# Kernel tuning notes

Measured on AMD Instinct MI355X. Metric: run time of the kernel, lower is better.

## Reference

```python
import jax, jax.numpy as jnp
import numpy as np

BIN = 256      # bin_num
DELTA = 0.01   # Huber delta
IM = 256       # imSize


def _soft_hist(u):
    # u: [B,H,W] values in [0,1]; BiasedConv1 with weight=1, bias_k = -(-1 + 2k/BIN)
    bias = 1.0 - 2.0 * jnp.arange(BIN, dtype=u.dtype) / BIN          # [BIN]
    a1 = u[:, None, :, :] + bias[None, :, None, None]                # [B,BIN,H,W]
    return jax.nn.relu(1.0 - jnp.abs(a1) * (BIN - 1))                # triangular kernel


def _hist2d(img):
    # img: [B,2,H,W] in [-1,1]
    ha = _soft_hist((img[:, 0] + 1.0) / 2.0)                         # [B,BIN,H,W]
    hb = _soft_hist((img[:, 1] + 1.0) / 2.0)                         # [B,BIN,H,W]
    H, W = img.shape[2], img.shape[3]
    # torch: repeat/repeat-view + elementwise mul + AvgPool2d(imSize)
    # == per-pixel outer product of (hb, ha) averaged over all pixels:
    # hist2d[b, j, r] = mean_hw hb[b,j,h,w] * ha[b,r,h,w]
    h2 = jnp.einsum('bjhw,brhw->bjr', hb, ha) / (H * W)              # [B,BIN,BIN]
    return h2[:, None]                                               # [B,1,BIN,BIN]


def reference(inp_image, ref_image):
    h_inp = _hist2d(inp_image)
    h_gt = _hist2d(ref_image)
    mann = jnp.abs(h_inp - h_gt)
    eucl = 0.5 * mann ** 2
    mask = (mann < DELTA).astype(mann.dtype)
    loss = eucl * mask / DELTA + (mann - 0.5 * DELTA) * (1.0 - mask)
    return jnp.sum(loss, axis=1, keepdims=True)                      # [B,1,BIN,BIN]


def setup_inputs() -> dict:
    key = jax.random.key(0)
    k1, k2 = jax.random.split(key)
    inp = jax.random.uniform(k1, (2, 2, IM, IM), dtype=jnp.float32) * 2.0 - 1.0
    ref = jax.random.uniform(k2, (2, 2, IM, IM), dtype=jnp.float32) * 2.0 - 1.0
    return {"inp_image": inp, "ref_image": ref}
```

## Files before the change

kernel.cpp:

```cpp
#include <hip/hip_runtime.h>


#define NPIX 65536
#define BINS 256
#define REPL 4
#define HSZ  (2 * NPIX)

__global__ void __launch_bounds__(256)
scatter_kernel(const float* __restrict__ inp,
               const float* __restrict__ ref,
               float* __restrict__ hist) {
    int gid = blockIdx.x * blockDim.x + threadIdx.x;
    int pix = gid & (NPIX - 1);
    int bb  = (gid >> 16) & 1;
    int im  = gid >> 17;
    const float* src = im ? ref : inp;
    float sgn = im ? -1.f : 1.f;
    float x0 = src[bb * (2 * NPIX) + pix];
    float x1 = src[bb * (2 * NPIX) + NPIX + pix];
    float* h = hist + (blockIdx.x & (REPL - 1)) * HSZ + bb * (BINS * BINS);

    float t0 = 64.f * x0 + 192.f;
    float t1 = 64.f * x1 + 192.f;
    int k0 = (int)floorf(t0);
    int k1 = (int)floorf(t1);

    float wr[2]; int ir[2]; int nr = 0;
    #pragma unroll
    for (int d = 0; d < 2; ++d) {
        int k = k0 + d;
        float w = 1.f - fabsf(t0 - (float)k) * 1.9921875f;
        if (w > 0.f && k >= 0 && k < BINS) { wr[nr] = w; ir[nr] = k; ++nr; }
    }
    float wj[2]; int ij[2]; int nj = 0;
    #pragma unroll
    for (int d = 0; d < 2; ++d) {
        int k = k1 + d;
        float w = 1.f - fabsf(t1 - (float)k) * 1.9921875f;
        if (w > 0.f && k >= 0 && k < BINS) { wj[nj] = w * sgn; ij[nj] = k; ++nj; }
    }
    for (int a = 0; a < nj; ++a)
        for (int b = 0; b < nr; ++b)
            atomicAdd(&h[ij[a] * BINS + ir[b]], wj[a] * wr[b]);
}

__global__ void __launch_bounds__(256)
loss_rezero_kernel(float* __restrict__ hist,
                   float* __restrict__ out) {
    int idx = blockIdx.x * blockDim.x + threadIdx.x;
    int bb = idx >> 16;
    int jr = idx & (NPIX - 1);
    float s = 0.f;
    #pragma unroll
    for (int r = 0; r < REPL; ++r) {
        float* p = &hist[r * HSZ + bb * (BINS * BINS) + jr];
        s += *p;
        *p = 0.f;
    }
    const float inv = 1.f / 65536.f;
    float mann = fabsf(s) * inv;
    float loss = (mann < 0.01f) ? (50.f * mann * mann) : (mann - 0.005f);
    out[idx] = loss;
}

extern "C" void kernel_launch(void* const* d_in, const int* in_sizes, int n_in,
                              void* d_out, int out_size, void* d_ws, size_t ws_size,
                              hipStream_t stream) {
    const float* inp = (const float*)d_in[0];
    const float* ref = (const float*)d_in[1];
    float* hist = (float*)d_ws;
    float* out  = (float*)d_out;

    scatter_kernel<<<(4 * NPIX) / 256, 256, 0, stream>>>(inp, ref, hist);
    loss_rezero_kernel<<<(2 * NPIX) / 256, 256, 0, stream>>>(hist, out);
}
```

Baseline: 69.71 us.

## Fuse scatter and loss kernels with a global atomic-counter grid barrier

Merges the histogram scatter and the loss/rezero pass into one kernel launch of 1024 blocks. A device-wide barrier built on a double-precision atomic counter with a generation target lets the first 512 blocks wait for all scatters before reducing the replicas, rezeroing them, and writing the loss. This removes one kernel launch and the inter-kernel gap. It relies on all 1024 blocks being co-resident, and it adds spin-wait and atomic overhead plus a guard-timeout that could yield wrong results if the barrier stalls.

```diff
diff --git a/kernel.cpp b/kernel.cpp
--- a/kernel.cpp
+++ b/kernel.cpp
@@ -5,12 +5,16 @@
 #define BINS 256
 #define REPL 4
 #define HSZ  (2 * NPIX)
+#define NBLK 1024
+#define NTHR 256
 
-__global__ void __launch_bounds__(256)
-scatter_kernel(const float* __restrict__ inp,
-               const float* __restrict__ ref,
-               float* __restrict__ hist) {
-    int gid = blockIdx.x * blockDim.x + threadIdx.x;
+__global__ void __launch_bounds__(NTHR, 4)
+fused_hist_loss_kernel(const float* __restrict__ inp,
+                       const float* __restrict__ ref,
+                       float* __restrict__ hist,
+                       double* __restrict__ cnt,
+                       float* __restrict__ out) {
+    int gid = blockIdx.x * NTHR + threadIdx.x;
     int pix = gid & (NPIX - 1);
     int bb  = (gid >> 16) & 1;
     int im  = gid >> 17;
@@ -42,25 +46,38 @@
     for (int a = 0; a < nj; ++a)
         for (int b = 0; b < nr; ++b)
             atomicAdd(&h[ij[a] * BINS + ir[b]], wj[a] * wr[b]);
-}
 
-__global__ void __launch_bounds__(256)
-loss_rezero_kernel(float* __restrict__ hist,
-                   float* __restrict__ out) {
-    int idx = blockIdx.x * blockDim.x + threadIdx.x;
-    int bb = idx >> 16;
-    int jr = idx & (NPIX - 1);
+    __threadfence();
+    __syncthreads();
+    if (threadIdx.x == 0) {
+        double old = atomicAdd(cnt, 1.0);
+        if (blockIdx.x < (2 * NPIX) / NTHR) {
+            double target = (floor((old + 0.5) * (1.0 / NBLK)) + 1.0) * (double)NBLK;
+            int guard = 0;
+            while (__hip_atomic_load(cnt, __ATOMIC_RELAXED,
+                                     __HIP_MEMORY_SCOPE_AGENT) < target) {
+                __builtin_amdgcn_s_sleep(1);
+                if (++guard > (1 << 22)) break;
+            }
+        }
+    }
+    __syncthreads();
+    if (blockIdx.x >= (2 * NPIX) / NTHR) return;
+    __threadfence();
+
+    int jr = gid & (NPIX - 1);
+    int b2 = gid >> 16;
     float s = 0.f;
     #pragma unroll
     for (int r = 0; r < REPL; ++r) {
-        float* p = &hist[r * HSZ + bb * (BINS * BINS) + jr];
-        s += *p;
-        *p = 0.f;
+        float* p = &hist[r * HSZ + b2 * (BINS * BINS) + jr];
+        s += __hip_atomic_load(p, __ATOMIC_RELAXED, __HIP_MEMORY_SCOPE_AGENT);
+        __hip_atomic_store(p, 0.f, __ATOMIC_RELAXED, __HIP_MEMORY_SCOPE_AGENT);
     }
     const float inv = 1.f / 65536.f;
     float mann = fabsf(s) * inv;
     float loss = (mann < 0.01f) ? (50.f * mann * mann) : (mann - 0.005f);
-    out[idx] = loss;
+    out[gid] = loss;
 }
 
 extern "C" void kernel_launch(void* const* d_in, const int* in_sizes, int n_in,
@@ -69,8 +86,8 @@
     const float* inp = (const float*)d_in[0];
     const float* ref = (const float*)d_in[1];
     float* hist = (float*)d_ws;
+    double* cnt = (double*)((char*)d_ws + REPL * HSZ * sizeof(float));
     float* out  = (float*)d_out;
 
-    scatter_kernel<<<(4 * NPIX) / 256, 256, 0, stream>>>(inp, ref, hist);
-    loss_rezero_kernel<<<(2 * NPIX) / 256, 256, 0, stream>>>(hist, out);
+    fused_hist_loss_kernel<<<NBLK, NTHR, 0, stream>>>(inp, ref, hist, cnt, out);
 }
```

New measurement: 174.2 us. +149.9%, slower.
